# Kernel tuning notes

Hardware: AMD Instinct MI355X
Metric: run time of the kernel (lower is better)

The kernel has to match this reference:

```python
import jax, jax.numpy as jnp
import numpy as np

DIST_THRESH = 150.0
ROW_EPS = 1e-6
BN_EPS = 1e-5


def setup_inputs() -> dict:
    key = jax.random.key(0)
    ks = jax.random.split(key, 6)
    B, N, T, D = 64, 64, 16, 512
    person_features = jax.random.normal(ks[0], (B, N, T, D), dtype=jnp.float32)
    # bboxes in pixel-ish units so the 150px threshold gives a mixed adjacency
    bboxes = jax.random.uniform(ks[1], (B, N, 4), dtype=jnp.float32) * 300.0
    w1 = jax.random.normal(ks[2], (D, D), dtype=jnp.float32) * (1.0 / np.sqrt(D))
    b1 = jax.random.normal(ks[3], (D,), dtype=jnp.float32) * 0.02
    w2 = jax.random.normal(ks[4], (D, D), dtype=jnp.float32) * (1.0 / np.sqrt(D))
    b2 = jax.random.normal(ks[5], (D,), dtype=jnp.float32) * 0.02
    g1 = jnp.ones((D,), jnp.float32); beta1 = jnp.zeros((D,), jnp.float32)
    g2 = jnp.ones((D,), jnp.float32); beta2 = jnp.zeros((D,), jnp.float32)
    return {"person_features": person_features, "bboxes": bboxes,
            "w1": w1, "b1": b1, "g1": g1, "beta1": beta1,
            "w2": w2, "b2": b2, "g2": g2, "beta2": beta2}


def _build_adjacency(bboxes):
    # centers: (B, N, 2) from x+w/2, y+h/2
    cx = bboxes[..., 0] + 0.5 * bboxes[..., 2]
    cy = bboxes[..., 1] + 0.5 * bboxes[..., 3]
    centers = jnp.stack([cx, cy], axis=-1)
    # pairwise distances (B, N, N), vectorized (replaces B*N*N python loop)
    diff = centers[:, :, None, :] - centers[:, None, :, :]
    dist = jnp.sqrt(jnp.sum(diff * diff, axis=-1))
    N = bboxes.shape[1]
    eye = jnp.eye(N, dtype=bboxes.dtype)
    off_diag = (eye[None] == 0.0)
    A = jnp.where((dist < DIST_THRESH) & off_diag, 1.0, 0.0) + eye[None]
    return A


def _stgcn(x, A, w, b, g, beta):
    # x: (B, N, C); A: (B, N, N)
    # torch: A_norm = A / (A.sum(dim=1 of A[i] -> axis=2) + eps)
    A_norm = A / (jnp.sum(A, axis=2, keepdims=True) + ROW_EPS)
    # x_graph = x[b].T @ A_norm[b]  -> (B, C, N)
    y = jnp.einsum('bnc,bnm->bcm', x, A_norm)
    # 1x1 conv == channel GEMM, bias added per out-channel
    y = jnp.einsum('oc,bcm->bom', w, y) + b[None, :, None]
    # BatchNorm2d in training mode: biased stats over (batch, spatial)
    mean = jnp.mean(y, axis=(0, 2), keepdims=True)
    var = jnp.mean(jnp.square(y - mean), axis=(0, 2), keepdims=True)
    y = (y - mean) / jnp.sqrt(var + BN_EPS)
    y = y * g[None, :, None] + beta[None, :, None]
    y = jax.nn.relu(y)
    return jnp.swapaxes(y, 1, 2)  # (B, N, C)


def reference(person_features, bboxes, w1, b1, g1, beta1, w2, b2, g2, beta2):
    A = _build_adjacency(bboxes)
    x = person_features[:, :, -1, :]  # (B, N, D) last frame
    h = _stgcn(x, A, w1, b1, g1, beta1)
    h = _stgcn(h, A, w2, b2, g2, beta2)
    # write enhanced features back into last timestep
    return person_features.at[:, :, -1, :].set(h)
```

## Files before the change

### kernel.cpp

```cpp
#include <hip/hip_runtime.h>
#include <hip/hip_bf16.h>


typedef __attribute__((ext_vector_type(8))) short short8;
typedef __attribute__((ext_vector_type(4))) float v4f;

#define DIST_THRESH 150.0f
#define ROW_EPS 1e-6f
#define BN_EPS 1e-5f

__device__ __forceinline__ ushort f2bf(float f) {
  union { __hip_bfloat16 h; ushort u; } cv;
  cv.h = __float2bfloat16(f);
  return cv.u;
}

__device__ __forceinline__ void copy_slab(const float4* __restrict__ in,
                                          float4* __restrict__ out,
                                          int blk, int t) {
  size_t base = (size_t)blk * 1024 + t;
  float4 r0 = in[base];
  float4 r1 = in[base + 256];
  float4 r2 = in[base + 512];
  float4 r3 = in[base + 768];
  out[base] = r0;
  out[base + 256] = r1;
  out[base + 512] = r2;
  out[base + 768] = r3;
}

__global__ __launch_bounds__(256) void k_agg(const float* __restrict__ Xbase,
                                             int rowStride,
                                             const float* __restrict__ bb,
                                             const float* __restrict__ stats,
                                             const float* __restrict__ g,
                                             const float* __restrict__ beta,
                                             int applyBN,
                                             ushort* __restrict__ Z,
                                             const float4* __restrict__ in4,
                                             float4* __restrict__ out4,
                                             int copyBase,
                                             int nonCopy,
                                             const float* __restrict__ w1,
                                             const float* __restrict__ w2,
                                             ushort* __restrict__ wb,
                                             float* __restrict__ statsZ) {
  int id = blockIdx.x;
  int t = threadIdx.x;

  if (id >= nonCopy) {
    copy_slab(in4, out4, copyBase + (id - nonCopy), t);
    return;
  }
  if (id >= 256) {
    int i4 = (id - 256) * 256 + t;
    float4 v = (i4 < 65536) ? *(const float4*)&w1[(size_t)i4 * 4]
                            : *(const float4*)&w2[(size_t)(i4 - 65536) * 4];
    ushort4 o;
    o.x = f2bf(v.x);
    o.y = f2bf(v.y);
    o.z = f2bf(v.z);
    o.w = f2bf(v.w);
    *(ushort4*)&wb[(size_t)i4 * 4] = o;
    if (i4 < 512) *(float4*)&statsZ[i4 * 4] = make_float4(0.f, 0.f, 0.f, 0.f);
    return;
  }

  int b = id >> 2;
  int c0 = (id & 3) << 7;
  __shared__ float Xs[64][128];
  __shared__ float As[64][64];
  __shared__ float cxs[64], cys[64];
  __shared__ float scaleS[128], shiftS[128];
  __shared__ float rsum[64][4];
  __shared__ float invr[64];

  if (t < 64) {
    float4 v = *(const float4*)&bb[(size_t)(b * 64 + t) * 4];
    cxs[t] = v.x + 0.5f * v.z;
    cys[t] = v.y + 0.5f * v.w;
  }
  if (applyBN && t < 32) {
    int c = t * 4;
    float4 sm = *(const float4*)&stats[c0 + c];
    float4 sq = *(const float4*)&stats[512 + c0 + c];
    float4 gg = *(const float4*)&g[c0 + c];
    float4 bt = *(const float4*)&beta[c0 + c];
    const float inv = 1.0f / 4096.0f;
    float mean, var, sc;
    mean = sm.x * inv; var = sq.x * inv - mean * mean; sc = gg.x * rsqrtf(var + BN_EPS);
    scaleS[c] = sc; shiftS[c] = bt.x - mean * sc;
    mean = sm.y * inv; var = sq.y * inv - mean * mean; sc = gg.y * rsqrtf(var + BN_EPS);
    scaleS[c + 1] = sc; shiftS[c + 1] = bt.y - mean * sc;
    mean = sm.z * inv; var = sq.z * inv - mean * mean; sc = gg.z * rsqrtf(var + BN_EPS);
    scaleS[c + 2] = sc; shiftS[c + 2] = bt.z - mean * sc;
    mean = sm.w * inv; var = sq.w * inv - mean * mean; sc = gg.w * rsqrtf(var + BN_EPS);
    scaleS[c + 3] = sc; shiftS[c + 3] = bt.w - mean * sc;
  }
  __syncthreads();

  int an = t >> 2, aq = t & 3;
  float av[16];
  {
    float mycx = cxs[an], mycy = cys[an];
    float ps = 0.f;
#pragma unroll
    for (int j = 0; j < 16; ++j) {
      int m = aq * 16 + j;
      float dx = mycx - cxs[m], dy = mycy - cys[m];
      float d = sqrtf(dx * dx + dy * dy);
      float a = (m == an) ? 1.0f : ((d < DIST_THRESH) ? 1.0f : 0.0f);
      av[j] = a;
      ps += a;
    }
    rsum[an][aq] = ps;
  }

  const float* xb = Xbase + (size_t)b * 64 * rowStride;
  for (int i = t; i < 2048; i += 256) {
    int n = i >> 5, c4 = (i & 31) << 2;
    float4 x = *(const float4*)&xb[(size_t)n * rowStride + c0 + c4];
    if (applyBN) {
      x.x = fmaxf(x.x * scaleS[c4] + shiftS[c4], 0.f);
      x.y = fmaxf(x.y * scaleS[c4 + 1] + shiftS[c4 + 1], 0.f);
      x.z = fmaxf(x.z * scaleS[c4 + 2] + shiftS[c4 + 2], 0.f);
      x.w = fmaxf(x.w * scaleS[c4 + 3] + shiftS[c4 + 3], 0.f);
    }
    *(float4*)&Xs[n][c4] = x;
  }
  __syncthreads();

  if (t < 64)
    invr[t] = 1.0f / (rsum[t][0] + rsum[t][1] + rsum[t][2] + rsum[t][3] + ROW_EPS);
  __syncthreads();

  {
    float iv = invr[an];
#pragma unroll
    for (int j = 0; j < 16; ++j) As[an][aq * 16 + j] = av[j] * iv;
  }
  __syncthreads();

  int c4 = (t & 31) << 2;
  int m0 = (t >> 5) << 3;
  float4 acc[8];
#pragma unroll
  for (int i = 0; i < 8; ++i) acc[i] = make_float4(0.f, 0.f, 0.f, 0.f);

  for (int n = 0; n < 64; ++n) {
    float4 x = *(const float4*)&Xs[n][c4];
    float4 a0 = *(const float4*)&As[n][m0];
    float4 a1 = *(const float4*)&As[n][m0 + 4];
    float as[8] = {a0.x, a0.y, a0.z, a0.w, a1.x, a1.y, a1.z, a1.w};
#pragma unroll
    for (int i = 0; i < 8; ++i) {
      acc[i].x = fmaf(as[i], x.x, acc[i].x);
      acc[i].y = fmaf(as[i], x.y, acc[i].y);
      acc[i].z = fmaf(as[i], x.z, acc[i].z);
      acc[i].w = fmaf(as[i], x.w, acc[i].w);
    }
  }

  size_t zbase = (size_t)b * 64 * 512 + c0 + c4;
#pragma unroll
  for (int i = 0; i < 8; ++i) {
    int m = m0 + i;
    ushort4 zz;
    zz.x = f2bf(acc[i].x);
    zz.y = f2bf(acc[i].y);
    zz.z = f2bf(acc[i].z);
    zz.w = f2bf(acc[i].w);
    *(ushort4*)&Z[zbase + (size_t)m * 512] = zz;
  }
}

__global__ __launch_bounds__(256) void k_gemm(const ushort* __restrict__ Z,
                                              const ushort* __restrict__ W,
                                              const float* __restrict__ bias,
                                              float* __restrict__ Y,
                                              float* __restrict__ sum,
                                              float* __restrict__ sumsq,
                                              const float4* __restrict__ in4,
                                              float4* __restrict__ out4,
                                              int copyBase) {
  int id = blockIdx.x;
  int t = threadIdx.x;
  if (id >= 512) {
    copy_slab(in4, out4, copyBase + (id - 512), t);
    return;
  }

  __shared__ __align__(16) ushort Zs[64 * 40];
  __shared__ __align__(16) ushort Ws[64 * 40];
  __shared__ float redS[4][64], redQ[4][64];

  int r0 = (id >> 3) << 6;
  int o0 = (id & 7) << 6;
  int wv = t >> 6, lane = t & 63;
  int m = lane & 15, q = lane >> 4;

  v4f acc[4];
#pragma unroll
  for (int nf = 0; nf < 4; ++nf) acc[nf] = (v4f){0.f, 0.f, 0.f, 0.f};

  int srow = t >> 2, scg = (t & 3) << 3;
  const ushort* zp = &Z[(size_t)(r0 + srow) * 512 + scg];
  const ushort* wp = &W[(size_t)(o0 + srow) * 512 + scg];

  uint4 zv = *(const uint4*)zp;
  uint4 wvv = *(const uint4*)wp;

  for (int ks = 0; ks < 16; ++ks) {
    __syncthreads();
    *(uint4*)&Zs[srow * 40 + scg] = zv;
    *(uint4*)&Ws[srow * 40 + scg] = wvv;
    __syncthreads();

    if (ks < 15) {
      zv = *(const uint4*)(zp + (ks + 1) * 32);
      wvv = *(const uint4*)(wp + (ks + 1) * 32);
    }

    short8 a = *(const short8*)&Zs[(wv * 16 + m) * 40 + q * 8];
#pragma unroll
    for (int nf = 0; nf < 4; ++nf) {
      short8 bfr = *(const short8*)&Ws[(nf * 16 + m) * 40 + q * 8];
      acc[nf] = __builtin_amdgcn_mfma_f32_16x16x32_bf16(a, bfr, acc[nf], 0, 0, 0);
    }
  }

#pragma unroll
  for (int nf = 0; nf < 4; ++nf) {
    int col = o0 + nf * 16 + m;
    float bv = bias[col];
    float s = 0.f, s2 = 0.f;
#pragma unroll
    for (int reg = 0; reg < 4; ++reg) {
      int row = r0 + wv * 16 + q * 4 + reg;
      float y = acc[nf][reg] + bv;
      Y[(size_t)row * 512 + col] = y;
      s += y;
      s2 += y * y;
    }
    s += __shfl_xor(s, 16);
    s += __shfl_xor(s, 32);
    s2 += __shfl_xor(s2, 16);
    s2 += __shfl_xor(s2, 32);
    if (q == 0) {
      redS[wv][nf * 16 + m] = s;
      redQ[wv][nf * 16 + m] = s2;
    }
  }
  __syncthreads();
  if (t < 64) {
    float s = redS[0][t] + redS[1][t] + redS[2][t] + redS[3][t];
    float s2 = redQ[0][t] + redQ[1][t] + redQ[2][t] + redQ[3][t];
    atomicAdd(&sum[o0 + t], s);
    atomicAdd(&sumsq[o0 + t], s2);
  }
}

__global__ __launch_bounds__(256) void k_norm(const float* __restrict__ Y,
                                              const float* __restrict__ sum,
                                              const float* __restrict__ sumsq,
                                              const float* __restrict__ g,
                                              const float* __restrict__ beta,
                                              float* __restrict__ out) {
  int idx = blockIdx.x * 256 + threadIdx.x;
  int o = (idx & 127) << 2;
  int r = idx >> 7;
  float4 y = *(const float4*)&Y[(size_t)r * 512 + o];
  float4 sm = *(const float4*)&sum[o];
  float4 sq = *(const float4*)&sumsq[o];
  float4 gg = *(const float4*)&g[o];
  float4 bb = *(const float4*)&beta[o];
  const float inv = 1.0f / 4096.0f;
  float4 h;
  {
    float mean = sm.x * inv, var = sq.x * inv - mean * mean;
    h.x = fmaxf(gg.x * (y.x - mean) * rsqrtf(var + BN_EPS) + bb.x, 0.f);
  }
  {
    float mean = sm.y * inv, var = sq.y * inv - mean * mean;
    h.y = fmaxf(gg.y * (y.y - mean) * rsqrtf(var + BN_EPS) + bb.y, 0.f);
  }
  {
    float mean = sm.z * inv, var = sq.z * inv - mean * mean;
    h.z = fmaxf(gg.z * (y.z - mean) * rsqrtf(var + BN_EPS) + bb.z, 0.f);
  }
  {
    float mean = sm.w * inv, var = sq.w * inv - mean * mean;
    h.w = fmaxf(gg.w * (y.w - mean) * rsqrtf(var + BN_EPS) + bb.w, 0.f);
  }
  *(float4*)&out[((size_t)r * 16 + 15) * 512 + o] = h;
}

extern "C" void kernel_launch(void* const* d_in, const int* in_sizes, int n_in,
                              void* d_out, int out_size, void* d_ws, size_t ws_size,
                              hipStream_t stream) {
  const float* pf = (const float*)d_in[0];
  const float* bboxes = (const float*)d_in[1];
  const float* w1 = (const float*)d_in[2];
  const float* b1 = (const float*)d_in[3];
  const float* g1 = (const float*)d_in[4];
  const float* be1 = (const float*)d_in[5];
  const float* w2 = (const float*)d_in[6];
  const float* b2 = (const float*)d_in[7];
  const float* g2 = (const float*)d_in[8];
  const float* be2 = (const float*)d_in[9];
  float* out = (float*)d_out;

  ushort* wb = (ushort*)d_ws;
  ushort* Zb = wb + 524288;
  float* Yb = (float*)(Zb + 2097152);
  float* stats = Yb + 2097152;
  float* sum1 = stats;
  float* sq1 = stats + 512;
  float* sum2 = stats + 1024;
  float* sq2 = stats + 1536;

  const float4* in4 = (const float4*)pf;
  float4* out4 = (float4*)out;

  k_agg<<<256 + 512 + 2048, 256, 0, stream>>>(pf + 7680, 8192, bboxes, stats,
                                              g1, be1, 0, Zb,
                                              in4, out4, 0, 768, w1, w2, wb, stats);
  k_gemm<<<512 + 2048, 256, 0, stream>>>(Zb, wb, b1, Yb, sum1, sq1,
                                         in4, out4, 2048);
  k_agg<<<256 + 2048, 256, 0, stream>>>(Yb, 512, bboxes, stats,
                                        g1, be1, 1, Zb,
                                        in4, out4, 4096, 256, w1, w2, wb, stats);
  k_gemm<<<512 + 2048, 256, 0, stream>>>(Zb, wb + 262144, b2, Yb, sum2, sq2,
                                         in4, out4, 6144);
  k_norm<<<2048, 256, 0, stream>>>(Yb, sum2, sq2, g2, be2, out);
}
```

Before: 280.2 us.

## Skip copying the overwritten last frame and rebalance copy blocks across kernels

The passthrough copy of person_features now works per (batch, person) group and copies only the first 15 timesteps. The last frame is skipped because k_norm overwrites it anyway, which cuts copy traffic by about one sixteenth. The copy blocks are redistributed across all five launches, including k_norm, so the bandwidth-bound copy overlaps with the compute stages more evenly. Weight bf16 conversion is coarsened to two units per block, and stats zeroing is confined to one block. The risks are uneven per-thread work (the conditional eighth load) and changed concurrency balance between the copy and the GEMM and aggregation blocks.

```diff
diff --git a/kernel.cpp b/kernel.cpp
--- a/kernel.cpp
+++ b/kernel.cpp
@@ -15,18 +15,31 @@
   return cv.u;
 }
 
-__device__ __forceinline__ void copy_slab(const float4* __restrict__ in,
-                                          float4* __restrict__ out,
-                                          int blk, int t) {
-  size_t base = (size_t)blk * 1024 + t;
-  float4 r0 = in[base];
-  float4 r1 = in[base + 256];
-  float4 r2 = in[base + 512];
-  float4 r3 = in[base + 768];
-  out[base] = r0;
-  out[base + 256] = r1;
-  out[base + 512] = r2;
-  out[base + 768] = r3;
+__device__ __forceinline__ void copy_group(const float4* __restrict__ in,
+                                           float4* __restrict__ out,
+                                           int g, int t) {
+  size_t base = (size_t)g * 2048 + t;
+  bool last = (t < 128);
+  float4 r[8];
+#pragma unroll
+  for (int k = 0; k < 7; ++k) r[k] = in[base + (size_t)k * 256];
+  if (last) r[7] = in[base + 7 * 256];
+#pragma unroll
+  for (int k = 0; k < 7; ++k) out[base + (size_t)k * 256] = r[k];
+  if (last) out[base + 7 * 256] = r[7];
+}
+
+__device__ __forceinline__ void prep_unit(int i4, const float* __restrict__ w1,
+                                          const float* __restrict__ w2,
+                                          ushort* __restrict__ wb) {
+  float4 v = (i4 < 65536) ? *(const float4*)&w1[(size_t)i4 * 4]
+                          : *(const float4*)&w2[(size_t)(i4 - 65536) * 4];
+  ushort4 o;
+  o.x = f2bf(v.x);
+  o.y = f2bf(v.y);
+  o.z = f2bf(v.z);
+  o.w = f2bf(v.w);
+  *(ushort4*)&wb[(size_t)i4 * 4] = o;
 }
 
 __global__ __launch_bounds__(256) void k_agg(const float* __restrict__ Xbase,
@@ -49,20 +62,17 @@
   int t = threadIdx.x;
 
   if (id >= nonCopy) {
-    copy_slab(in4, out4, copyBase + (id - nonCopy), t);
+    copy_group(in4, out4, copyBase + (id - nonCopy), t);
     return;
   }
   if (id >= 256) {
-    int i4 = (id - 256) * 256 + t;
-    float4 v = (i4 < 65536) ? *(const float4*)&w1[(size_t)i4 * 4]
-                            : *(const float4*)&w2[(size_t)(i4 - 65536) * 4];
-    ushort4 o;
-    o.x = f2bf(v.x);
-    o.y = f2bf(v.y);
-    o.z = f2bf(v.z);
-    o.w = f2bf(v.w);
-    *(ushort4*)&wb[(size_t)i4 * 4] = o;
-    if (i4 < 512) *(float4*)&statsZ[i4 * 4] = make_float4(0.f, 0.f, 0.f, 0.f);
+    int pb = id - 256;
+#pragma unroll
+    for (int u = 0; u < 2; ++u) prep_unit((pb * 2 + u) * 256 + t, w1, w2, wb);
+    if (pb == 0) {
+      for (int i = t; i < 512; i += 256)
+        ((float4*)statsZ)[i] = make_float4(0.f, 0.f, 0.f, 0.f);
+    }
     return;
   }
 
@@ -186,7 +196,7 @@
   int id = blockIdx.x;
   int t = threadIdx.x;
   if (id >= 512) {
-    copy_slab(in4, out4, copyBase + (id - 512), t);
+    copy_group(in4, out4, copyBase + (id - 512), t);
     return;
   }
 
@@ -265,8 +275,17 @@
                                               const float* __restrict__ sumsq,
                                               const float* __restrict__ g,
                                               const float* __restrict__ beta,
-                                              float* __restrict__ out) {
-  int idx = blockIdx.x * 256 + threadIdx.x;
+                                              float* __restrict__ out,
+                                              const float4* __restrict__ in4,
+                                              float4* __restrict__ out4,
+                                              int copyBase) {
+  int id = blockIdx.x;
+  int t = threadIdx.x;
+  if (id >= 2048) {
+    copy_group(in4, out4, copyBase + (id - 2048), t);
+    return;
+  }
+  int idx = id * 256 + t;
   int o = (idx & 127) << 2;
   int r = idx >> 7;
   float4 y = *(const float4*)&Y[(size_t)r * 512 + o];
@@ -322,15 +341,17 @@
   const float4* in4 = (const float4*)pf;
   float4* out4 = (float4*)out;
 
-  k_agg<<<256 + 512 + 2048, 256, 0, stream>>>(pf + 7680, 8192, bboxes, stats,
-                                              g1, be1, 0, Zb,
-                                              in4, out4, 0, 768, w1, w2, wb, stats);
-  k_gemm<<<512 + 2048, 256, 0, stream>>>(Zb, wb, b1, Yb, sum1, sq1,
-                                         in4, out4, 2048);
-  k_agg<<<256 + 2048, 256, 0, stream>>>(Yb, 512, bboxes, stats,
-                                        g1, be1, 1, Zb,
-                                        in4, out4, 4096, 256, w1, w2, wb, stats);
-  k_gemm<<<512 + 2048, 256, 0, stream>>>(Zb, wb + 262144, b2, Yb, sum2, sq2,
-                                         in4, out4, 6144);
-  k_norm<<<2048, 256, 0, stream>>>(Yb, sum2, sq2, g2, be2, out);
-}
+
+  k_agg<<<256 + 256 + 512, 256, 0, stream>>>(pf + 7680, 8192, bboxes, stats,
+                                             g1, be1, 0, Zb,
+                                             in4, out4, 0, 512, w1, w2, wb, stats);
+  k_gemm<<<512 + 896, 256, 0, stream>>>(Zb, wb, b1, Yb, sum1, sq1,
+                                        in4, out4, 512);
+  k_agg<<<256 + 512, 256, 0, stream>>>(Yb, 512, bboxes, stats,
+                                       g1, be1, 1, Zb,
+                                       in4, out4, 1408, 256, w1, w2, wb, stats);
+  k_gemm<<<512 + 896, 256, 0, stream>>>(Zb, wb + 262144, b2, Yb, sum2, sq2,
+                                        in4, out4, 1920);
+  k_norm<<<2048 + 1280, 256, 0, stream>>>(Yb, sum2, sq2, g2, be2, out,
+                                          in4, out4, 2816);
+}
```

Result: slower. 290.4 us (+3.7%).
